# Performance work log

Measured on AMD Instinct MI355X. Metric: run time of the kernel, lower is better.

Reference implementation:

```python
import jax, jax.numpy as jnp
import numpy as np

B, H, C, D, HID = 32, 100, 50, 400, 400


def setup_inputs() -> dict:
    key = jax.random.key(0)
    k0, k1, k2, k3, k4, k5 = jax.random.split(key, 6)
    hist_news_vector = jax.random.normal(k0, (B, H, D), jnp.float32)
    cand_news_vector = jax.random.normal(k1, (B, C, D), jnp.float32)
    mask_hist = jax.random.bernoulli(k2, 0.9, (B, H))
    mask_cand = jax.random.bernoulli(k3, 0.9, (B, C))
    # dnn params: Linear(2D -> HID) then Linear(HID -> 1) (no activation in between, as in source)
    W1 = (jax.random.normal(k4, (2 * D, HID), jnp.float32) * 0.02)
    b1 = jnp.zeros((HID,), jnp.float32)
    w2 = (jax.random.normal(k5, (HID,), jnp.float32) * 0.02)
    b2 = jnp.zeros((), jnp.float32)
    return dict(hist_news_vector=hist_news_vector, cand_news_vector=cand_news_vector,
                mask_hist=mask_hist, mask_cand=mask_cand, W1=W1, b1=b1, w2=w2, b2=b2)


def reference(hist_news_vector, cand_news_vector, mask_hist, mask_cand, W1, b1, w2, b2):
    d = cand_news_vector.shape[-1]
    # concat order in source is [cand, hist]; split W1 so we never materialize the [B,C,H,2D] concat
    W1c, W1h = W1[:d], W1[d:]
    cand_part = cand_news_vector @ W1c            # [B, C, HID]
    hist_part = hist_news_vector @ W1h            # [B, H, HID]
    h = cand_part[:, :, None, :] + hist_part[:, None, :, :] + b1   # [B, C, H, HID]
    scores = h @ w2 + b2                          # [B, C, H]
    neg = jnp.finfo(scores.dtype).min
    scores = jnp.where(mask_hist[:, None, :], scores, neg)
    weights = jax.nn.softmax(scores, axis=-1)     # softmax over hist dim
    weights = jnp.where(mask_cand[:, :, None], weights, jnp.zeros((), weights.dtype))
    user_vector = jnp.einsum('bch,bhd->bcd', weights, hist_news_vector)  # [B, C, D]
    return user_vector
```

## Files before the change

kernel.cpp:

```cpp
#include <hip/hip_runtime.h>
#include <math.h>

#define B_   32
#define H_   100
#define C_   50
#define D_   400
#define HID_ 400
#define ROWS (B_ * H_)
#define T_   7
#define RCH  32

#define NEGF (-3.4028234663852886e38f)


__device__ __forceinline__ float wave_reduce_add(float v) {
    #pragma unroll
    for (int off = 32; off; off >>= 1) v += __shfl_xor(v, off, 64);
    return v;
}

__global__ __launch_bounds__(512)
void k_scores(const float* __restrict__ hist,
              const float* __restrict__ W1,
              const float* __restrict__ w2,
              float* __restrict__ s_part) {
    __shared__ float4 u4_lds[16];

    const int t    = blockIdx.x >> 5;
    const int r    = blockIdx.x & 31;
    const int d0   = t * 64;
    const int dt   = (d0 + 64 <= D_) ? 64 : (D_ - d0);
    const int lane = threadIdx.x & 63;
    const int wave = threadIdx.x >> 6;

    const float4* w24 = (const float4*)w2;
    for (int i = wave; i < dt; i += 8) {
        const float4* row4 = (const float4*)(W1 + (size_t)(D_ + d0 + i) * HID_);
        float4 a0 = row4[lane], b0 = w24[lane];
        float acc = a0.x*b0.x + a0.y*b0.y + a0.z*b0.z + a0.w*b0.w;
        if (lane < 36) {
            float4 a1 = row4[64 + lane], b1 = w24[64 + lane];
            acc += a1.x*b1.x + a1.y*b1.y + a1.z*b1.z + a1.w*b1.w;
        }
        acc = wave_reduce_add(acc);
        if (lane == 0) ((float*)u4_lds)[i] = acc;
    }
    __syncthreads();

    const int l16 = lane & 15;
    const int sub = lane >> 4;
    const int dt4 = dt >> 2;
    const float4 uu = (l16 < dt4) ? u4_lds[l16] : make_float4(0.f,0.f,0.f,0.f);
    const float4* h4 = (const float4*)hist;
    float* sp = s_part + (size_t)t * ROWS;
    const int row0 = r * 100;
    #pragma unroll
    for (int p = 0; p < 4; p++) {
        const int rl = p * 32 + wave * 4 + sub;
        if (rl < 100) {
            const int row = row0 + rl;
            float4 a = (l16 < dt4) ? h4[(size_t)row * 100 + t * 16 + l16]
                                   : make_float4(0.f,0.f,0.f,0.f);
            float acc = a.x*uu.x + a.y*uu.y + a.z*uu.z + a.w*uu.w;
            #pragma unroll
            for (int off = 8; off; off >>= 1)
                acc += __shfl_xor(acc, off, 64);
            if (l16 == 0) sp[row] = acc;
        }
    }
}

__global__ __launch_bounds__(256)
void k_out(const float* __restrict__ hist, const float* __restrict__ s_part,
           const int* __restrict__ mask_hist, const int* __restrict__ mask_cand,
           float* __restrict__ out) {
    __shared__ float s_lds[H_];
    __shared__ float w_lds[H_];
    __shared__ float part[4][64];

    const int b    = blockIdx.x / T_;
    const int tile = blockIdx.x % T_;
    const int d0   = tile * 64;
    const int lane = threadIdx.x & 63;
    const int wave = threadIdx.x >> 6;
    const int tid  = threadIdx.x;

    if (tid < H_) {
        const int row = b * H_ + tid;
        float sum = 0.f;
        #pragma unroll
        for (int t = 0; t < T_; t++) sum += s_part[(size_t)t * ROWS + row];
        s_lds[tid] = mask_hist[row] ? sum : NEGF;
    }
    __syncthreads();

    const float s0 = s_lds[lane];
    const float s1 = (lane < 36) ? s_lds[64 + lane] : -INFINITY;
    float m = fmaxf(s0, s1);
    #pragma unroll
    for (int off = 32; off; off >>= 1) m = fmaxf(m, __shfl_xor(m, off, 64));
    const float e0 = expf(s0 - m);
    const float e1 = (lane < 36) ? expf(s1 - m) : 0.f;
    const float inv = 1.f / wave_reduce_add(e0 + e1);
    if (wave == 0) {
        w_lds[lane] = e0 * inv;
        if (lane < 36) w_lds[64 + lane] = e1 * inv;
    }
    __syncthreads();

    const float* hb = hist + (size_t)b * H_ * D_;
    const int d = d0 + lane;
    float acc = 0.f;
    if (d < D_) {
        const int h0 = wave * 25;
        #pragma unroll
        for (int i = 0; i < 25; i++)
            acc = fmaf(w_lds[h0 + i], hb[(size_t)(h0 + i) * D_ + d], acc);
    }
    part[wave][lane] = acc;
    __syncthreads();

    const float uv = part[0][lane] + part[1][lane] + part[2][lane] + part[3][lane];
    const int* mc  = mask_cand + b * C_;
    float* outb = out + (size_t)b * C_ * D_ + d0;
    if (d < D_) {
        for (int c = wave; c < C_; c += 4)
            outb[(size_t)c * D_ + lane] = mc[c] ? uv : 0.f;
    }
}

extern "C" void kernel_launch(void* const* d_in, const int* in_sizes, int n_in,
                              void* d_out, int out_size, void* d_ws, size_t ws_size,
                              hipStream_t stream) {
    const float* hist      = (const float*)d_in[0];
    const int*   mask_hist = (const int*)d_in[2];
    const int*   mask_cand = (const int*)d_in[3];
    const float* W1        = (const float*)d_in[4];
    const float* w2        = (const float*)d_in[6];
    float* out = (float*)d_out;

    float* s_part = (float*)d_ws;

    k_scores<<<T_ * RCH, 512, 0, stream>>>(hist, W1, w2, s_part);
    k_out   <<<B_ * T_,  256, 0, stream>>>(hist, s_part, mask_hist, mask_cand, out);
}
```

Measured before the change: 16.63 us.

## Prefetch hist loads before dependent reductions and pack partial scores per row

In k_scores, the hist tile loads are issued before the W1·w2 reduction so their latency overlaps with it. That reduction now uses 16-lane groups computing 32 rows at once instead of full waves. Partial scores are stored row-major with a stride of 8, so k_out can sum them with two float4 loads. k_out also preloads its 25 hist values into registers before the softmax and uses two accumulators. The cost is higher register pressure and stores from lanes that are later masked out.

```diff
diff --git a/kernel.cpp b/kernel.cpp
--- a/kernel.cpp
+++ b/kernel.cpp
@@ -8,15 +8,13 @@
 #define HID_ 400
 #define ROWS (B_ * H_)
 #define T_   7
-#define RCH  32
+#define SPLD 8
 
 #define NEGF (-3.4028234663852886e38f)
 
 
-__device__ __forceinline__ float wave_reduce_add(float v) {
-    #pragma unroll
-    for (int off = 32; off; off >>= 1) v += __shfl_xor(v, off, 64);
-    return v;
+__device__ __forceinline__ float dot4(float4 a, float4 b) {
+    return fmaf(a.x, b.x, fmaf(a.y, b.y, fmaf(a.z, b.z, a.w * b.w)));
 }
 
 __global__ __launch_bounds__(512)
@@ -24,49 +22,61 @@
               const float* __restrict__ W1,
               const float* __restrict__ w2,
               float* __restrict__ s_part) {
-    __shared__ float4 u4_lds[16];
+    __shared__ float u_lds[64];
 
     const int t    = blockIdx.x >> 5;
     const int r    = blockIdx.x & 31;
     const int d0   = t * 64;
-    const int dt   = (d0 + 64 <= D_) ? 64 : (D_ - d0);
-    const int lane = threadIdx.x & 63;
-    const int wave = threadIdx.x >> 6;
+    const int dt   = (t < 6) ? 64 : 16;
+    const int dt4  = dt >> 2;
+    const int tid  = threadIdx.x;
+    const int lane = tid & 63;
+    const int wave = tid >> 6;
+    const int l16  = lane & 15;
+    const int sub  = lane >> 4;
+    const int g    = tid >> 4;
+
+    const float4* h4 = (const float4*)hist;
+    const bool cload = (l16 < dt4);
+    float4 ha[4];
+    int   rown[4];
+    #pragma unroll
+    for (int p = 0; p < 4; p++) {
+        const int rl = p * 32 + wave * 4 + sub;
+        rown[p] = r * 100 + rl;
+        ha[p] = (rl < 100 && cload)
+              ? h4[(size_t)rown[p] * 100 + t * 16 + l16]
+              : make_float4(0.f, 0.f, 0.f, 0.f);
+    }
 
     const float4* w24 = (const float4*)w2;
-    for (int i = wave; i < dt; i += 8) {
+    #pragma unroll 2
+    for (int i = g; i < dt; i += 32) {
         const float4* row4 = (const float4*)(W1 + (size_t)(D_ + d0 + i) * HID_);
-        float4 a0 = row4[lane], b0 = w24[lane];
-        float acc = a0.x*b0.x + a0.y*b0.y + a0.z*b0.z + a0.w*b0.w;
-        if (lane < 36) {
-            float4 a1 = row4[64 + lane], b1 = w24[64 + lane];
-            acc += a1.x*b1.x + a1.y*b1.y + a1.z*b1.z + a1.w*b1.w;
-        }
-        acc = wave_reduce_add(acc);
-        if (lane == 0) ((float*)u4_lds)[i] = acc;
+        float acc = 0.f;
+        #pragma unroll
+        for (int k = 0; k < 6; k++)
+            acc += dot4(row4[l16 + 16 * k], w24[l16 + 16 * k]);
+        if (l16 < 4)
+            acc += dot4(row4[96 + l16], w24[96 + l16]);
+        #pragma unroll
+        for (int off = 8; off; off >>= 1)
+            acc += __shfl_xor(acc, off, 64);
+        if (l16 == 0) u_lds[i] = acc;
     }
     __syncthreads();
 
-    const int l16 = lane & 15;
-    const int sub = lane >> 4;
-    const int dt4 = dt >> 2;
-    const float4 uu = (l16 < dt4) ? u4_lds[l16] : make_float4(0.f,0.f,0.f,0.f);
-    const float4* h4 = (const float4*)hist;
-    float* sp = s_part + (size_t)t * ROWS;
-    const int row0 = r * 100;
+    const float4 uu = cload ? ((const float4*)u_lds)[l16]
+                            : make_float4(0.f, 0.f, 0.f, 0.f);
     #pragma unroll
     for (int p = 0; p < 4; p++) {
         const int rl = p * 32 + wave * 4 + sub;
-        if (rl < 100) {
-            const int row = row0 + rl;
-            float4 a = (l16 < dt4) ? h4[(size_t)row * 100 + t * 16 + l16]
-                                   : make_float4(0.f,0.f,0.f,0.f);
-            float acc = a.x*uu.x + a.y*uu.y + a.z*uu.z + a.w*uu.w;
-            #pragma unroll
-            for (int off = 8; off; off >>= 1)
-                acc += __shfl_xor(acc, off, 64);
-            if (l16 == 0) sp[row] = acc;
-        }
+        float acc = dot4(ha[p], uu);
+        #pragma unroll
+        for (int off = 8; off; off >>= 1)
+            acc += __shfl_xor(acc, off, 64);
+        if (rl < 100 && l16 == 0)
+            s_part[(size_t)rown[p] * SPLD + t] = acc;
     }
 }
 
@@ -75,7 +85,6 @@
            const int* __restrict__ mask_hist, const int* __restrict__ mask_cand,
            float* __restrict__ out) {
     __shared__ float s_lds[H_];
-    __shared__ float w_lds[H_];
     __shared__ float part[4][64];
 
     const int b    = blockIdx.x / T_;
@@ -84,12 +93,21 @@
     const int lane = threadIdx.x & 63;
     const int wave = threadIdx.x >> 6;
     const int tid  = threadIdx.x;
+    const int d    = d0 + lane;
+    const bool dv  = (d < D_);
+
+    const float* hb = hist + (size_t)b * H_ * D_;
+    const int h0 = wave * 25;
+    float r[25];
+    #pragma unroll
+    for (int i = 0; i < 25; i++)
+        r[i] = dv ? hb[(size_t)(h0 + i) * D_ + d] : 0.f;
 
     if (tid < H_) {
         const int row = b * H_ + tid;
-        float sum = 0.f;
-        #pragma unroll
-        for (int t = 0; t < T_; t++) sum += s_part[(size_t)t * ROWS + row];
+        const float4* sp4 = (const float4*)(s_part + (size_t)row * SPLD);
+        float4 a = sp4[0], c = sp4[1];
+        float sum = ((a.x + a.y) + (a.z + a.w)) + ((c.x + c.y) + c.z);
         s_lds[tid] = mask_hist[row] ? sum : NEGF;
     }
     __syncthreads();
@@ -101,29 +119,30 @@
     for (int off = 32; off; off >>= 1) m = fmaxf(m, __shfl_xor(m, off, 64));
     const float e0 = expf(s0 - m);
     const float e1 = (lane < 36) ? expf(s1 - m) : 0.f;
-    const float inv = 1.f / wave_reduce_add(e0 + e1);
+    float ps = e0 + e1;
+    #pragma unroll
+    for (int off = 32; off; off >>= 1) ps += __shfl_xor(ps, off, 64);
+    const float inv = 1.f / ps;
     if (wave == 0) {
-        w_lds[lane] = e0 * inv;
-        if (lane < 36) w_lds[64 + lane] = e1 * inv;
+        s_lds[lane] = e0 * inv;
+        if (lane < 36) s_lds[64 + lane] = e1 * inv;
     }
     __syncthreads();
 
-    const float* hb = hist + (size_t)b * H_ * D_;
-    const int d = d0 + lane;
-    float acc = 0.f;
-    if (d < D_) {
-        const int h0 = wave * 25;
-        #pragma unroll
-        for (int i = 0; i < 25; i++)
-            acc = fmaf(w_lds[h0 + i], hb[(size_t)(h0 + i) * D_ + d], acc);
+    float acc0 = 0.f, acc1 = 0.f;
+    #pragma unroll
+    for (int i = 0; i < 24; i += 2) {
+        acc0 = fmaf(s_lds[h0 + i],     r[i],     acc0);
+        acc1 = fmaf(s_lds[h0 + i + 1], r[i + 1], acc1);
     }
-    part[wave][lane] = acc;
+    acc0 = fmaf(s_lds[h0 + 24], r[24], acc0);
+    part[wave][lane] = acc0 + acc1;
     __syncthreads();
 
     const float uv = part[0][lane] + part[1][lane] + part[2][lane] + part[3][lane];
     const int* mc  = mask_cand + b * C_;
     float* outb = out + (size_t)b * C_ * D_ + d0;
-    if (d < D_) {
+    if (dv) {
         for (int c = wave; c < C_; c += 4)
             outb[(size_t)c * D_ + lane] = mc[c] ? uv : 0.f;
     }
@@ -141,6 +160,6 @@
 
     float* s_part = (float*)d_ws;
 
-    k_scores<<<T_ * RCH, 512, 0, stream>>>(hist, W1, w2, s_part);
-    k_out   <<<B_ * T_,  256, 0, stream>>>(hist, s_part, mask_hist, mask_cand, out);
+    k_scores<<<T_ * 32, 512, 0, stream>>>(hist, W1, w2, s_part);
+    k_out   <<<B_ * T_, 256, 0, stream>>>(hist, s_part, mask_hist, mask_cand, out);
 }
```

New measurement: 14.68 us. -11.7%, faster.
